# Kernel optimization log

Hardware: AMD Instinct MI355X
Metric: run time of the kernel (lower is better)

## Reference

```python
import jax, jax.numpy as jnp
import numpy as np

EMO = 1024
FEAT = 1024
K = 128  # aggregation_k
H_LIST = (4, 8, 16)
D_LIST = tuple(EMO // h for h in H_LIST)  # (256, 128, 64)
D_SUM = sum(D_LIST)  # 448
H_SUM = sum(H_LIST)  # 28
N = len(H_LIST)      # 3 subspaces
TEMP = float(np.power(D_SUM, 0.5))


def _block_mask(sizes, total):
    m = np.zeros((len(sizes), total), np.float32)
    off = 0
    for i, s in enumerate(sizes):
        m[i, off:off + s] = 1.0
        off += s
    return jnp.asarray(m)

M_Q_BLK = _block_mask(D_LIST, D_SUM)  # [N, d_sum]
M_V_BLK = _block_mask(H_LIST, H_SUM)  # [N, h_sum]


def setup_inputs() -> dict:
    key = jax.random.key(0)
    ks = iter(jax.random.split(key, 32))
    nrm = lambda shape, s=1.0: jax.random.normal(next(ks), shape, jnp.float32) * s
    B, Lt, Lp, Nv = 32, 1024, 512, 256
    return {
        "emo_embedding": nrm((B, Lt, EMO)),
        "phr_feat": nrm((B, Lp, FEAT)),
        "video_feat": nrm((B, Nv, FEAT)),
        "w_v_W": nrm((FEAT, FEAT), FEAT ** -0.5), "w_v_b": nrm((FEAT,), 0.01),
        "agg_a_W": nrm((FEAT, K), FEAT ** -0.5), "agg_a_b": nrm((K,), 0.01),
        "agg_c_W": nrm((FEAT, EMO), FEAT ** -0.5), "agg_c_b": nrm((EMO,), 0.01),
        "ele_W": nrm((2 * EMO, 1), (2 * EMO) ** -0.5), "ele_b": nrm((1,), 0.01),
        "wq_W": nrm((EMO, D_SUM), EMO ** -0.5), "wq_b": nrm((D_SUM,), 0.01),
        "wk_W": nrm((EMO, D_SUM), EMO ** -0.5), "wk_b": nrm((D_SUM,), 0.01),
        "wv_W": nrm((EMO, H_SUM), EMO ** -0.5), "wv_b": nrm((H_SUM,), 0.01),
        "wr_W": nrm((EMO, N), EMO ** -0.5), "wr_b": nrm((N,), 0.01),
    }


def reference(emo_embedding, phr_feat, video_feat,
              w_v_W, w_v_b, agg_a_W, agg_a_b, agg_c_W, agg_c_b,
              ele_W, ele_b, wq_W, wq_b, wk_W, wk_b, wv_W, wv_b, wr_W, wr_b):
    B, Lt, _ = emo_embedding.shape
    Nv = video_feat.shape[1]
    Lp = phr_feat.shape[1]

    # --- feature_aggregation ---
    # AdaptiveAvgPool1d(Nv); Lp % Nv == 0 so it is an exact reshape-mean.
    phr = phr_feat.reshape(B, Nv, Lp // Nv, FEAT).mean(axis=2)
    combine = jnp.concatenate([phr @ w_v_W + w_v_b, video_feat], axis=1)   # [B, 2*Nv, FEAT]
    attn_a = jax.nn.softmax(combine @ agg_a_W + agg_a_b, axis=-1)          # [B, 2*Nv, K]
    agg_feat = jnp.einsum('bmk,bme->bke', attn_a, combine @ agg_c_W + agg_c_b)  # [B, K, EMO]

    # --- element_routing ---
    A_pool = jnp.einsum('ble,bke->blk', emo_embedding, agg_feat).mean(axis=1)   # [B, K]
    route = jnp.einsum('bk,bke->be', A_pool, agg_feat)[:, None, :]              # [B, 1, EMO]
    route = jnp.broadcast_to(route, emo_embedding.shape)
    R_e = jnp.tanh(jnp.concatenate([emo_embedding, route], axis=-1) @ ele_W + ele_b)  # [B, Lt, 1]
    route_emo = R_e * emo_embedding                                              # [B, Lt, EMO]

    # --- subspace_routing ---
    Q = route_emo @ wq_W + wq_b        # [B, Lt, d_sum]
    Kp = agg_feat @ wk_W + wk_b        # [B, K, d_sum]
    V = agg_feat @ wv_W + wv_b         # [B, K, h_sum]
    Rp = agg_feat @ wr_W + wr_b        # [B, K, N]

    # N masked copies of Q (block subspace masks); K/R are plain repeats, V is masked.
    Qm = (Q[:, None] * M_Q_BLK[None, :, None, :]).reshape(B, N * Lt, D_SUM)
    Kf = jnp.tile(Kp, (1, N, 1))                                         # [B, N*K, d_sum]
    Vf = (V[:, None] * M_V_BLK[None, :, None, :]).reshape(B, N * K, H_SUM)
    Rf = jnp.tile(Rp, (1, N, 1))                                         # [B, N*K, N]

    attn = jax.nn.softmax(jnp.einsum('bqd,bkd->bqk', Qm, Kf) / TEMP, axis=-1)  # [B, N*Lt, N*K]
    O = jnp.tanh(attn @ Vf).reshape(B, N, Lt, H_SUM)
    O_R = (attn @ Rf).reshape(B, N, Lt, N)

    # per-subspace head gating of route_emo
    T_list = []
    hoff = 0
    for i in range(N):
        hi, di = H_LIST[i], D_LIST[i]
        ori = route_emo.reshape(B, Lt, hi, di)
        Oi = O[:, i, :, hoff:hoff + hi][..., None]      # [B, Lt, hi, 1]
        T_list.append((ori * Oi).reshape(B, Lt, EMO))
        hoff += hi
    T = jnp.stack(T_list, axis=1)                        # [B, N, Lt, EMO]

    Rdiag = jnp.stack([O_R[:, j, :, j].mean(axis=-1) for j in range(N)], axis=1)  # [B, N]
    gate = jax.nn.softmax(Rdiag, axis=-1)[:, :, None, None]
    return emo_embedding + (gate * T).sum(axis=1)
```

## Files before the change

### kernel.cpp

```cpp
#include <hip/hip_runtime.h>
#include <math.h>

typedef long long i64;
typedef __attribute__((ext_vector_type(8))) short bf16x8;
typedef __attribute__((ext_vector_type(4))) float f32x4;

#define TEMP_ISQ 0.047245559f

__device__ __forceinline__ unsigned short f2b(float x) {
  union { float f; unsigned u; } a; a.f = x;
  return (unsigned short)((a.u + 0x7fffu + ((a.u >> 16) & 1u)) >> 16);
}
__device__ __forceinline__ float b2f(unsigned short b) {
  union { float f; unsigned u; } a; a.u = ((unsigned)b) << 16; return a.f;
}

template<int BIAS, int OUTM, int RS, int BZDIV, int XMODE = 0>
__global__ __launch_bounds__(256)
void gemm_mfma(const unsigned short* __restrict__ Ab, i64 sA,
               const unsigned short* __restrict__ Bb, i64 sB,
               const float* __restrict__ bias,
               void* __restrict__ Ob, i64 sO,
               unsigned short* __restrict__ O2b, i64 sO2,
               int Nn, int Kd, int ldA, int ldB, int ldO,
               const float* __restrict__ rowScale, i64 sRS,
               const float* __restrict__ rsAdd)
{
  __shared__ unsigned short As[2][4096];
  __shared__ unsigned short Bs[2][4096];
  const int tid = threadIdx.x;
  const int w = tid >> 6, lane = tid & 63;

  const int gx = gridDim.x, gy = gridDim.y;
  int nwg = gx * gy * gridDim.z;
  int bid = blockIdx.x + gx * (blockIdx.y + gy * blockIdx.z);
  int L = bid;
  if ((nwg & 7) == 0) L = (bid & 7) * (nwg >> 3) + (bid >> 3);
  const int bx = L % gx;
  int rem = L / gx;
  const int by = rem % gy;
  const int z  = rem / gy;

  const int m0 = by * 128, n0 = bx * 128;
  int zA = (XMODE == 2) ? z / 3 : z;
  const unsigned short* A;
  const unsigned short* B;
  int KdL = Kd;
  if (XMODE == 3) {
    int bb = z / 3, ii = z - bb * 3;
    const int dof_[3] = {0, 256, 384};
    const int kdt_[3] = {256, 128, 64};
    A = Ab + (i64)bb * sA + dof_[ii];
    B = Bb + dof_[ii];
    KdL = kdt_[ii];
  } else if (XMODE == 2) {
    A = Ab + (i64)zA * sA;
    B = Bb + (i64)z * sB;
  } else {
    A = Ab + (i64)z * sA;
    B = Bb + (i64)(BZDIV == 1 ? z : z / BZDIV) * sB;
  }
  const int wr = w >> 1, wc = w & 1;
  const int rS = tid >> 2, sS = tid & 3;
  const int cL = lane & 15, sl = lane >> 4;

  f32x4 acc[4][4];
  #pragma unroll
  for (int i = 0; i < 4; ++i)
    #pragma unroll
    for (int j = 0; j < 4; ++j) acc[i][j] = (f32x4){0.f, 0.f, 0.f, 0.f};

  auto STAGE = [&](int buf, int k0) {
    #pragma unroll
    for (int q = 0; q < 2; ++q) {
      int r = rS + q * 64;
      int sg = sS ^ ((r >> 1) & 3);
      const unsigned short* sa = A + (i64)(m0 + r) * ldA + k0 + sg * 8;
      const unsigned short* sb = B + (i64)(n0 + r) * ldB + k0 + sg * 8;
      __builtin_amdgcn_global_load_lds(
          (__attribute__((address_space(1))) void*)sa,
          (__attribute__((address_space(3))) void*)&As[buf][r * 32 + sS * 8], 16, 0, 0);
      __builtin_amdgcn_global_load_lds(
          (__attribute__((address_space(1))) void*)sb,
          (__attribute__((address_space(3))) void*)&Bs[buf][r * 32 + sS * 8], 16, 0, 0);
    }
  };

  STAGE(0, 0);
  __syncthreads();

  for (int k0 = 0; k0 < KdL; k0 += 32) {
    const int cur = (k0 >> 5) & 1;
    if (k0 + 32 < KdL) STAGE(cur ^ 1, k0 + 32);
    bf16x8 af[4], bfv[4];
    #pragma unroll
    for (int mi = 0; mi < 4; ++mi) {
      int rr = wr * 64 + mi * 16 + cL;
      int ph = sl ^ ((rr >> 1) & 3);
      af[mi] = *(const bf16x8*)&As[cur][rr * 32 + ph * 8];
    }
    #pragma unroll
    for (int ni = 0; ni < 4; ++ni) {
      int rr = wc * 64 + ni * 16 + cL;
      int ph = sl ^ ((rr >> 1) & 3);
      bfv[ni] = *(const bf16x8*)&Bs[cur][rr * 32 + ph * 8];
    }
    #pragma unroll
    for (int mi = 0; mi < 4; ++mi)
      #pragma unroll
      for (int ni = 0; ni < 4; ++ni)
        acc[mi][ni] = __builtin_amdgcn_mfma_f32_16x16x32_bf16(af[mi], bfv[ni], acc[mi][ni], 0, 0, 0);
    __syncthreads();
  }

  const float* bp = (XMODE == 2) ? (bias + (i64)z * 128) : bias;
  #pragma unroll
  for (int mi = 0; mi < 4; ++mi) {
    const int rowb = m0 + wr * 64 + mi * 16 + sl * 4;
    #pragma unroll
    for (int ni = 0; ni < 4; ++ni) {
      const int col = n0 + wc * 64 + ni * 16 + cL;
      if (col < Nn) {
        float bc = (BIAS == 1) ? bp[col] : 0.f;
        #pragma unroll
        for (int rg = 0; rg < 4; ++rg) {
          float v = acc[mi][ni][rg];
          if (RS) v *= tanhf(rowScale[(i64)zA * sRS + rowb + rg] + rsAdd[zA]);
          v += bc;
          if (BIAS == 2) v += bias[rowb + rg];
          i64 oidx = (i64)(rowb + rg) * ldO + col;
          if (OUTM == 0)      ((float*)Ob)[(i64)z * sO + oidx] = v;
          else if (OUTM == 1) ((unsigned short*)Ob)[(i64)z * sO + oidx] = f2b(v);
          else if (OUTM == 4) {
            float ov = (col < 28) ? tanhf(v * (1.f / 3.f)) : v * (1.f / 1024.f);
            ((float*)Ob)[(i64)z * sO + oidx] = ov;
          } else {
            ((float*)Ob)[(i64)z * sO + oidx] = v;
            O2b[(i64)z * sO2 + oidx] = f2b(v);
          }
        }
      }
    }
  }
}

__global__ __launch_bounds__(256)
void emo_pass1(const float* __restrict__ emo, const float* __restrict__ eleW,
               unsigned short* __restrict__ emoB, float* __restrict__ colPart,
               float* __restrict__ dotE) {
  int b = blockIdx.y, lc = blockIdx.x;
  int t = threadIdx.x, lane = t & 63, w = t >> 6;
  float4 w4 = ((const float4*)eleW)[t];
  float4 acc = make_float4(0.f, 0.f, 0.f, 0.f);
  __shared__ float dw[16][4];
  const float4* src = (const float4*)emo + ((i64)b * 1024 + lc * 16) * 256;
  ushort4* dst = (ushort4*)emoB + ((i64)b * 1024 + lc * 16) * 256;
  #pragma unroll 4
  for (int lr = 0; lr < 16; ++lr) {
    float4 v = src[lr * 256 + t];
    acc.x += v.x; acc.y += v.y; acc.z += v.z; acc.w += v.w;
    float d = v.x * w4.x + v.y * w4.y + v.z * w4.z + v.w * w4.w;
    #pragma unroll
    for (int o = 32; o; o >>= 1) d += __shfl_xor(d, o);
    if (!lane) dw[lr][w] = d;
    ushort4 o4; o4.x = f2b(v.x); o4.y = f2b(v.y); o4.z = f2b(v.z); o4.w = f2b(v.w);
    dst[lr * 256 + t] = o4;
  }
  __syncthreads();
  if (t < 16) dotE[(i64)b * 1024 + lc * 16 + t] = dw[t][0] + dw[t][1] + dw[t][2] + dw[t][3];
  ((float4*)colPart)[((i64)b * 64 + lc) * 256 + t] = acc;
}

__global__ __launch_bounds__(256)
void transpose_all(const float* __restrict__ w_v_W, const float* __restrict__ agg_a_W,
                   const float* __restrict__ agg_c_W, const float* __restrict__ wq_W,
                   const float* __restrict__ wk_W, const float* __restrict__ wv_W,
                   const float* __restrict__ wr_W,
                   unsigned short* __restrict__ wvT, unsigned short* __restrict__ aaT,
                   unsigned short* __restrict__ acT, unsigned short* __restrict__ wqB,
                   unsigned short* __restrict__ kvrT) {
  int bx = blockIdx.x;
  int t = threadIdx.x;
  if (bx >= 84) {
    i64 li = (((i64)(bx - 84) * 32 + blockIdx.y) * 256 + t) * 4;
    float4 v = *(const float4*)(wq_W + li);
    ushort4 o; o.x = f2b(v.x); o.y = f2b(v.y); o.z = f2b(v.z); o.w = f2b(v.w);
    *(ushort4*)(wqB + li) = o;
    return;
  }
  __shared__ float T[32][33];
  const float* in; unsigned short* out; int N, Npad, s0;
  if (bx < 32)      { in = w_v_W;   out = wvT;                     N = 1024; Npad = 1024; s0 = 0; }
  else if (bx < 36) { in = agg_a_W; out = aaT;                     N = 128;  Npad = 128;  s0 = 32; }
  else if (bx < 68) { in = agg_c_W; out = acT;                     N = 1024; Npad = 1024; s0 = 36; }
  else if (bx < 82) { in = wk_W;    out = kvrT;                    N = 448;  Npad = 448;  s0 = 68; }
  else if (bx < 83) { in = wv_W;    out = kvrT + (i64)448 * 1024;  N = 28;   Npad = 28;   s0 = 82; }
  else              { in = wr_W;    out = kvrT + (i64)476 * 1024;  N = 3;    Npad = 36;   s0 = 83; }
  int n0 = (bx - s0) * 32, k0 = blockIdx.y * 32;
  #pragma unroll
  for (int p = 0; p < 4; ++p) {
    int idx = t + 256 * p; int kk = idx >> 5, nn = idx & 31;
    float v = 0.f;
    if (n0 + nn < N) v = in[(i64)(k0 + kk) * N + (n0 + nn)];
    T[nn][kk] = v;
  }
  __syncthreads();
  #pragma unroll
  for (int p = 0; p < 4; ++p) {
    int idx = t + 256 * p; int nn = idx >> 5, kk = idx & 31;
    if (n0 + nn < Npad) out[(i64)(n0 + nn) * 1024 + (k0 + kk)] = f2b(T[nn][kk]);
  }
}

__global__ void kvr_bias_kernel(const float* wkb, const float* wvb, const float* wrb, float* out) {
  int t = blockIdx.x * 256 + threadIdx.x;
  if (t >= 480) return;
  out[t] = (t < 448) ? wkb[t] : (t < 476) ? wvb[t - 448] : (t < 479) ? wrb[t - 476] : 0.f;
}

__global__ void pv_conv(const float* __restrict__ phr, const float* __restrict__ video,
                        unsigned short* __restrict__ pooled, unsigned short* __restrict__ combine) {
  i64 idx = (i64)blockIdx.x * 256 + threadIdx.x;
  if (idx < 2097152) {
    i64 bm = idx >> 8; int c = (int)(idx & 255);
    i64 b = bm >> 8, m = bm & 255;
    const float4* r0 = (const float4*)(phr + (b * 512 + 2 * m) * 1024) + c;
    const float4* r1 = (const float4*)(phr + (b * 512 + 2 * m + 1) * 1024) + c;
    float4 a = *r0, d = *r1;
    ushort4 o;
    o.x = f2b(0.5f * (a.x + d.x)); o.y = f2b(0.5f * (a.y + d.y));
    o.z = f2b(0.5f * (a.z + d.z)); o.w = f2b(0.5f * (a.w + d.w));
    ((ushort4*)pooled)[idx] = o;
  } else {
    i64 j = idx - 2097152;
    i64 b = j >> 16, r = j & 65535;
    float4 v = ((const float4*)video)[j];
    ushort4 o;
    o.x = f2b(v.x); o.y = f2b(v.y); o.z = f2b(v.z); o.w = f2b(v.w);
    ((ushort4*)combine)[b * 131072 + 65536 + r] = o;
  }
}

__global__ void vtq_fill(const unsigned short* __restrict__ KVR, const float* __restrict__ wq_b,
                         unsigned short* __restrict__ VT, float* __restrict__ qb) {
  int b = blockIdx.y, bx = blockIdx.x, t = threadIdx.x;
  if (bx < 64) {
    int idx = bx * 256 + t;
    int n = idx >> 7, k = idx & 127;
    unsigned short v = 0;
    if (n < 28)      v = KVR[(i64)b * 61440 + k * 480 + 448 + n];
    else if (n < 31) v = KVR[(i64)b * 61440 + k * 480 + 476 + (n - 28)];
    VT[((i64)b * 128 + n) * 128 + k] = v;
  } else if (t < 128) {
    int ii = bx - 64;
    const int dof_[3] = {0, 256, 384};
    const int kdt_[3] = {256, 128, 64};
    const unsigned short* kp = KVR + (i64)b * 61440 + t * 480 + dof_[ii];
    const float* wb = wq_b + dof_[ii];
    float s = 0.f;
    for (int d = 0; d < kdt_[ii]; ++d) s += b2f(kp[d]) * wb[d];
    qb[(b * 3 + ii) * 128 + t] = s;
  }
}

__global__ void softmax_attn_a(const float* __restrict__ logits, unsigned short* __restrict__ outT) {
  int gw = (int)(((i64)blockIdx.x * blockDim.x + threadIdx.x) >> 6);
  int lane = threadIdx.x & 63;
  if (gw >= 32 * 512) return;
  int b = gw >> 9, m = gw & 511;
  const float* p = logits + (i64)gw * 128;
  float x0 = p[lane], x1 = p[lane + 64];
  float mx = fmaxf(x0, x1);
  #pragma unroll
  for (int o = 32; o; o >>= 1) mx = fmaxf(mx, __shfl_xor(mx, o));
  float e0 = expf(x0 - mx), e1 = expf(x1 - mx);
  float s = e0 + e1;
  #pragma unroll
  for (int o = 32; o; o >>= 1) s += __shfl_xor(s, o);
  float inv = 1.f / s;
  unsigned short* o0 = outT + (i64)b * 128 * 512 + m;
  o0[(i64)lane * 512] = f2b(e0 * inv);
  o0[(i64)(lane + 64) * 512] = f2b(e1 * inv);
}

__global__ void softmax_P_bf(const unsigned short* __restrict__ PL, unsigned short* __restrict__ P) {
  i64 gw = ((i64)blockIdx.x * blockDim.x + threadIdx.x) >> 6;
  int lane = threadIdx.x & 63;
  if (gw >= 98304) return;
  const unsigned short* p = PL + gw * 128;
  float x0 = b2f(p[lane]) * TEMP_ISQ, x1 = b2f(p[lane + 64]) * TEMP_ISQ;
  float mx = fmaxf(x0, x1);
  #pragma unroll
  for (int o = 32; o; o >>= 1) mx = fmaxf(mx, __shfl_xor(mx, o));
  float e0 = expf(x0 - mx), e1 = expf(x1 - mx);
  float s = e0 + e1;
  #pragma unroll
  for (int o = 32; o; o >>= 1) s += __shfl_xor(s, o);
  float inv = 1.f / s;
  P[gw * 128 + lane] = f2b(e0 * inv);
  P[gw * 128 + lane + 64] = f2b(e1 * inv);
}

__global__ __launch_bounds__(256)
void colmean_apool(const float* __restrict__ colPart, const float* __restrict__ aggF,
                   float* __restrict__ Apool) {
  int b = blockIdx.x, t = threadIdx.x, lane = t & 63, w = t >> 6;
  __shared__ float em[1024];
  float4 s = make_float4(0.f, 0.f, 0.f, 0.f);
  const float4* cp = (const float4*)colPart + (i64)b * 64 * 256 + t;
  for (int lc = 0; lc < 64; ++lc) {
    float4 v = cp[lc * 256];
    s.x += v.x; s.y += v.y; s.z += v.z; s.w += v.w;
  }
  em[t * 4 + 0] = s.x * (1.f / 1024.f); em[t * 4 + 1] = s.y * (1.f / 1024.f);
  em[t * 4 + 2] = s.z * (1.f / 1024.f); em[t * 4 + 3] = s.w * (1.f / 1024.f);
  __syncthreads();
  for (int k = w; k < 128; k += 4) {
    const float* ag = aggF + ((i64)b * 128 + k) * 1024;
    float d = 0.f;
    #pragma unroll
    for (int j = 0; j < 16; ++j) { int e = j * 64 + lane; d += em[e] * ag[e]; }
    #pragma unroll
    for (int o = 32; o; o >>= 1) d += __shfl_down(d, o);
    if (!lane) Apool[b * 128 + k] = d;
  }
}

__global__ __launch_bounds__(256)
void route_rb(const float* __restrict__ Apool, const float* __restrict__ aggF,
              const float* __restrict__ eleW, const float* __restrict__ eleb,
              float* __restrict__ rbv) {
  int b = blockIdx.x, t = threadIdx.x;
  __shared__ float Ap[128];
  if (t < 128) Ap[t] = Apool[b * 128 + t];
  __syncthreads();
  float4 r = make_float4(0.f, 0.f, 0.f, 0.f);
  const float4* ag = (const float4*)(aggF + (i64)b * 128 * 1024) + t;
  #pragma unroll 8
  for (int k = 0; k < 128; ++k) {
    float a = Ap[k];
    float4 v = ag[(i64)k * 256];
    r.x += a * v.x; r.y += a * v.y; r.z += a * v.z; r.w += a * v.w;
  }
  float4 w4 = ((const float4*)(eleW + 1024))[t];
  float d = r.x * w4.x + r.y * w4.y + r.z * w4.z + r.w * w4.w;
  __shared__ float red[256];
  red[t] = d; __syncthreads();
  for (int o = 128; o > 0; o >>= 1) { if (t < o) red[t] += red[t + o]; __syncthreads(); }
  if (t == 0) rbv[b] = red[0] + eleb[0];
}

__global__ void gate_kernel(const float* __restrict__ O, float* __restrict__ gate) {
  int b = blockIdx.x, t = threadIdx.x;
  __shared__ float red[128];
  __shared__ float rd[3];
  for (int i = 0; i < 3; ++i) {
    const float* op = O + ((i64)(b * 3 + i) * 1024) * 32 + 28 + i;
    float s = 0.f;
    #pragma unroll
    for (int l = t; l < 1024; l += 128) s += op[(i64)l * 32];
    red[t] = s; __syncthreads();
    for (int o = 64; o > 0; o >>= 1) { if (t < o) red[t] += red[t + o]; __syncthreads(); }
    if (t == 0) rd[i] = red[0];
    __syncthreads();
  }
  if (t == 0) {
    float m = fmaxf(rd[0], fmaxf(rd[1], rd[2]));
    float e0 = expf(rd[0] - m), e1 = expf(rd[1] - m), e2 = expf(rd[2] - m);
    float inv = 1.f / (e0 + e1 + e2);
    gate[b * 3 + 0] = e0 * inv; gate[b * 3 + 1] = e1 * inv; gate[b * 3 + 2] = e2 * inv;
  }
}

__global__ __launch_bounds__(256)
void final_kernel(const unsigned short* __restrict__ emoB, const float* __restrict__ dotE,
                  const float* __restrict__ rbv, const float* __restrict__ O,
                  const float* __restrict__ gate, float* __restrict__ out) {
  i64 bl = blockIdx.x;
  int b = (int)(bl >> 10), l = (int)(bl & 1023);
  __shared__ float Gg[16];
  int t = threadIdx.x;
  if (t < 16) {
    float g0 = gate[b * 3], g1 = gate[b * 3 + 1], g2 = gate[b * 3 + 2];
    float o0 = O[((i64)(b * 3 + 0) * 1024 + l) * 32 + (t >> 2)];
    float o1 = O[((i64)(b * 3 + 1) * 1024 + l) * 32 + 4 + (t >> 1)];
    float o2 = O[((i64)(b * 3 + 2) * 1024 + l) * 32 + 12 + t];
    Gg[t] = g0 * o0 + g1 * o1 + g2 * o2;
  }
  __syncthreads();
  float re = tanhf(dotE[bl] + rbv[b]);
  ushort4 e4 = ((const ushort4*)(emoB + bl * 1024))[t];
  float g = 1.f + re * Gg[t >> 4];
  ((float4*)(out + bl * 1024))[t] =
      make_float4(b2f(e4.x) * g, b2f(e4.y) * g, b2f(e4.z) * g, b2f(e4.w) * g);
}

extern "C" void kernel_launch(void* const* d_in, const int* in_sizes, int n_in,
                              void* d_out, int out_size, void* d_ws, size_t ws_size,
                              hipStream_t stream) {
  const float* emo     = (const float*)d_in[0];
  const float* phr     = (const float*)d_in[1];
  const float* video   = (const float*)d_in[2];
  const float* w_v_W   = (const float*)d_in[3];
  const float* w_v_b   = (const float*)d_in[4];
  const float* agg_a_W = (const float*)d_in[5];
  const float* agg_a_b = (const float*)d_in[6];
  const float* agg_c_W = (const float*)d_in[7];
  const float* agg_c_b = (const float*)d_in[8];
  const float* ele_W   = (const float*)d_in[9];
  const float* ele_b   = (const float*)d_in[10];
  const float* wq_W    = (const float*)d_in[11];
  const float* wq_b    = (const float*)d_in[12];
  const float* wk_W    = (const float*)d_in[13];
  const float* wk_b    = (const float*)d_in[14];
  const float* wv_W    = (const float*)d_in[15];
  const float* wv_b    = (const float*)d_in[16];
  const float* wr_W    = (const float*)d_in[17];
  const float* wr_b    = (const float*)d_in[18];

  char* ws = (char*)d_ws;
  const i64 oEmoB    = 0;
  const i64 oCombine = 67108864;
  const i64 oP       = 67108864;
  const i64 oPooled  = 100663296;
  const i64 oLogitsA = 100663296;
  const i64 oAggF    = 100663296;
  const i64 oO       = 100663296;
  const i64 oCT      = 117440512;
  const i64 oW2T     = 117440512;
  const i64 oAttnAT  = 150994944;
  const i64 oAggB    = 155189248;
  const i64 oWvT     = 163577856;
  const i64 oAaT     = 165675008;
  const i64 oAcT     = 165937152;
  const i64 oWqB     = 168034304;
  const i64 oKvrT    = 169082880;
  const i64 oKVR     = 170131456;
  const i64 oVT      = 174063616;
  const i64 oKvrB    = 175112192;
  const i64 oColPart = 175247360;
  const i64 oDotE    = 183635968;
  const i64 oApool   = 183767040;
  const i64 oQb      = 183783424;
  const i64 oRb      = 183914496;
  const i64 oGate    = 184307968;

  unsigned short* emoB    = (unsigned short*)(ws + oEmoB);
  unsigned short* combine = (unsigned short*)(ws + oCombine);
  unsigned short* P       = (unsigned short*)(ws + oP);
  unsigned short* pooled  = (unsigned short*)(ws + oPooled);
  float*          logitsA = (float*)(ws + oLogitsA);
  float*          aggF    = (float*)(ws + oAggF);
  float*          O       = (float*)(ws + oO);
  unsigned short* CT      = (unsigned short*)(ws + oCT);
  unsigned short* W2T     = (unsigned short*)(ws + oW2T);
  unsigned short* attnAT  = (unsigned short*)(ws + oAttnAT);
  unsigned short* aggB    = (unsigned short*)(ws + oAggB);
  unsigned short* wvT     = (unsigned short*)(ws + oWvT);
  unsigned short* aaT     = (unsigned short*)(ws + oAaT);
  unsigned short* acT     = (unsigned short*)(ws + oAcT);
  unsigned short* wqB     = (unsigned short*)(ws + oWqB);
  unsigned short* kvrT    = (unsigned short*)(ws + oKvrT);
  unsigned short* KVR     = (unsigned short*)(ws + oKVR);
  unsigned short* VT      = (unsigned short*)(ws + oVT);
  float*          kvrB    = (float*)(ws + oKvrB);
  float*          colPart = (float*)(ws + oColPart);
  float*          dotE    = (float*)(ws + oDotE);
  float*          Apool   = (float*)(ws + oApool);
  float*          qb      = (float*)(ws + oQb);
  float*          rbv     = (float*)(ws + oRb);
  float*          gate    = (float*)(ws + oGate);

  dim3 blk(256);

  emo_pass1<<<dim3(64, 32), blk, 0, stream>>>(emo, ele_W, emoB, colPart, dotE);

  transpose_all<<<dim3(98, 32), blk, 0, stream>>>(w_v_W, agg_a_W, agg_c_W, wq_W, wk_W, wv_W, wr_W,
                                                  wvT, aaT, acT, wqB, kvrT);
  kvr_bias_kernel<<<2, blk, 0, stream>>>(wk_b, wv_b, wr_b, kvrB);

  pv_conv<<<16384, blk, 0, stream>>>(phr, video, pooled, combine);
  gemm_mfma<1, 1, 0, 1><<<dim3(8, 2, 32), blk, 0, stream>>>(pooled, 262144, wvT, 0, w_v_b,
      (void*)combine, 524288, nullptr, 0, 1024, 1024, 1024, 1024, 1024, nullptr, 0, nullptr);
  gemm_mfma<1, 0, 0, 1><<<dim3(1, 4, 32), blk, 0, stream>>>(combine, 524288, aaT, 0, agg_a_b,
      (void*)logitsA, 65536, nullptr, 0, 128, 1024, 1024, 1024, 128, nullptr, 0, nullptr);
  softmax_attn_a<<<4096, blk, 0, stream>>>(logitsA, attnAT);
  gemm_mfma<2, 1, 0, 1><<<dim3(4, 8, 32), blk, 0, stream>>>(acT, 0, combine, 524288, agg_c_b,
      (void*)CT, 524288, nullptr, 0, 512, 1024, 1024, 1024, 512, nullptr, 0, nullptr);
  gemm_mfma<0, 2, 0, 1><<<dim3(8, 1, 32), blk, 0, stream>>>(attnAT, 65536, CT, 524288, nullptr,
      (void*)aggF, 131072, aggB, 131072, 1024, 512, 512, 512, 1024, nullptr, 0, nullptr);

  colmean_apool<<<32, blk, 0, stream>>>(colPart, aggF, Apool);
  route_rb<<<32, blk, 0, stream>>>(Apool, aggF, ele_W, ele_b, rbv);

  gemm_mfma<1, 1, 0, 1><<<dim3(4, 1, 32), blk, 0, stream>>>(aggB, 131072, kvrT, 0, kvrB,
      (void*)KVR, 61440, nullptr, 0, 480, 1024, 1024, 1024, 480, nullptr, 0, nullptr);
  vtq_fill<<<dim3(67, 32), blk, 0, stream>>>(KVR, wq_b, VT, qb);

  gemm_mfma<0, 1, 0, 1, 3><<<dim3(8, 1, 96), blk, 0, stream>>>(KVR, 61440, wqB, 0, nullptr,
      (void*)W2T, 131072, nullptr, 0, 1024, 0, 480, 448, 1024, nullptr, 0, nullptr);

  gemm_mfma<1, 1, 1, 1, 2><<<dim3(1, 8, 96), blk, 0, stream>>>(emoB, 1048576, W2T, 131072, qb,
      (void*)P, 131072, nullptr, 0, 128, 1024, 1024, 1024, 128, dotE, 1024, rbv);

  softmax_P_bf<<<24576, blk, 0, stream>>>(P, P);

  gemm_mfma<0, 4, 0, 3><<<dim3(1, 8, 96), blk, 0, stream>>>(P, 131072, VT, 16384, nullptr,
      (void*)O, 32768, nullptr, 0, 31, 128, 128, 128, 32, nullptr, 0, nullptr);

  gate_kernel<<<32, 128, 0, stream>>>(O, gate);
  final_kernel<<<32768, blk, 0, stream>>>(emoB, dotE, rbv, O, gate, (float*)d_out);
}
```

Measured before the change: 458.1 us.

## Reassociate aggregation einsum to apply attention before the agg_c projection

Computes agg_feat as (attn_a^T @ combine) @ agg_c_W + colsum(attn_a) * agg_c_b instead of attn_a^T @ (combine @ agg_c_W + b). This shrinks the large projection GEMM from 512 rows per batch to 128 rows per batch. To support it, the change adds a combine transpose kernel, a column-sum kernel for the bias term, and a new BIAS mode that scales the bias by a per-row factor. The intermediate S1 is rounded to bf16, which slightly changes numerics.

Measured after the change: 450.8 us (median of 2 runs). No clear change (-1.6%).

```diff
diff --git a/kernel.cpp b/kernel.cpp
--- a/kernel.cpp
+++ b/kernel.cpp
@@ -128,6 +128,7 @@
           if (RS) v *= tanhf(rowScale[(i64)zA * sRS + rowb + rg] + rsAdd[zA]);
           v += bc;
           if (BIAS == 2) v += bias[rowb + rg];
+          if (BIAS == 3) v += rowScale[(i64)z * sRS + rowb + rg] * bp[col];
           i64 oidx = (i64)(rowb + rg) * ldO + col;
           if (OUTM == 0)      ((float*)Ob)[(i64)z * sO + oidx] = v;
           else if (OUTM == 1) ((unsigned short*)Ob)[(i64)z * sO + oidx] = f2b(v);
@@ -239,6 +240,41 @@
     o.x = f2b(v.x); o.y = f2b(v.y); o.z = f2b(v.z); o.w = f2b(v.w);
     ((ushort4*)combine)[b * 131072 + 65536 + r] = o;
   }
+}
+
+__global__ __launch_bounds__(256)
+void combT_kernel(const unsigned short* __restrict__ in, unsigned short* __restrict__ out) {
+  __shared__ unsigned short T[64][68];
+  int b = blockIdx.z, mt = blockIdx.y, ft = blockIdx.x;
+  int t = threadIdx.x;
+  const unsigned short* src = in + (i64)b * 524288 + (i64)(mt * 64) * 1024 + ft * 64;
+  unsigned short* dst = out + (i64)b * 524288 + (i64)(ft * 64) * 512 + mt * 64;
+  int r0 = t >> 4, c4 = (t & 15) * 4;
+  #pragma unroll
+  for (int p = 0; p < 4; ++p) {
+    int r = r0 + p * 16;
+    ushort4 v = *(const ushort4*)&src[(i64)r * 1024 + c4];
+    T[r][c4] = v.x; T[r][c4 + 1] = v.y; T[r][c4 + 2] = v.z; T[r][c4 + 3] = v.w;
+  }
+  __syncthreads();
+  #pragma unroll
+  for (int p = 0; p < 4; ++p) {
+    int fr = r0 + p * 16;
+    ushort4 v;
+    v.x = T[c4][fr]; v.y = T[c4 + 1][fr]; v.z = T[c4 + 2][fr]; v.w = T[c4 + 3][fr];
+    *(ushort4*)&dst[(i64)fr * 512 + c4] = v;
+  }
+}
+
+__global__ void colsum_kernel(const unsigned short* __restrict__ attnAT, float* __restrict__ colsum) {
+  int b = blockIdx.x, k = threadIdx.x;
+  const ushort4* p = (const ushort4*)(attnAT + ((i64)b * 128 + k) * 512);
+  float s = 0.f;
+  for (int m4 = 0; m4 < 128; ++m4) {
+    ushort4 v = p[m4];
+    s += b2f(v.x) + b2f(v.y) + b2f(v.z) + b2f(v.w);
+  }
+  colsum[b * 128 + k] = s;
 }
 
 __global__ void vtq_fill(const unsigned short* __restrict__ KVR, const float* __restrict__ wq_b,
@@ -421,6 +457,7 @@
   char* ws = (char*)d_ws;
   const i64 oEmoB    = 0;
   const i64 oCombine = 67108864;
+  const i64 oS1B     = 67108864;
   const i64 oP       = 67108864;
   const i64 oPooled  = 100663296;
   const i64 oLogitsA = 100663296;
@@ -444,15 +481,17 @@
   const i64 oQb      = 183783424;
   const i64 oRb      = 183914496;
   const i64 oGate    = 184307968;
+  const i64 oColsum  = 184308480;
 
   unsigned short* emoB    = (unsigned short*)(ws + oEmoB);
   unsigned short* combine = (unsigned short*)(ws + oCombine);
+  unsigned short* S1B     = (unsigned short*)(ws + oS1B);
   unsigned short* P       = (unsigned short*)(ws + oP);
   unsigned short* pooled  = (unsigned short*)(ws + oPooled);
   float*          logitsA = (float*)(ws + oLogitsA);
   float*          aggF    = (float*)(ws + oAggF);
   float*          O       = (float*)(ws + oO);
-  unsigned short* CT      = (unsigned short*)(ws + oCT);
+  unsigned short* combineT= (unsigned short*)(ws + oCT);
   unsigned short* W2T     = (unsigned short*)(ws + oW2T);
   unsigned short* attnAT  = (unsigned short*)(ws + oAttnAT);
   unsigned short* aggB    = (unsigned short*)(ws + oAggB);
@@ -470,6 +509,7 @@
   float*          qb      = (float*)(ws + oQb);
   float*          rbv     = (float*)(ws + oRb);
   float*          gate    = (float*)(ws + oGate);
+  float*          colsum  = (float*)(ws + oColsum);
 
   dim3 blk(256);
 
@@ -485,10 +525,13 @@
   gemm_mfma<1, 0, 0, 1><<<dim3(1, 4, 32), blk, 0, stream>>>(combine, 524288, aaT, 0, agg_a_b,
       (void*)logitsA, 65536, nullptr, 0, 128, 1024, 1024, 1024, 128, nullptr, 0, nullptr);
   softmax_attn_a<<<4096, blk, 0, stream>>>(logitsA, attnAT);
-  gemm_mfma<2, 1, 0, 1><<<dim3(4, 8, 32), blk, 0, stream>>>(acT, 0, combine, 524288, agg_c_b,
-      (void*)CT, 524288, nullptr, 0, 512, 1024, 1024, 1024, 512, nullptr, 0, nullptr);
-  gemm_mfma<0, 2, 0, 1><<<dim3(8, 1, 32), blk, 0, stream>>>(attnAT, 65536, CT, 524288, nullptr,
-      (void*)aggF, 131072, aggB, 131072, 1024, 512, 512, 512, 1024, nullptr, 0, nullptr);
+  colsum_kernel<<<32, 128, 0, stream>>>(attnAT, colsum);
+  combT_kernel<<<dim3(16, 8, 32), blk, 0, stream>>>(combine, combineT);
+
+  gemm_mfma<0, 1, 0, 1><<<dim3(8, 1, 32), blk, 0, stream>>>(attnAT, 65536, combineT, 524288, nullptr,
+      (void*)S1B, 131072, nullptr, 0, 1024, 512, 512, 512, 1024, nullptr, 0, nullptr);
+  gemm_mfma<3, 2, 0, 1><<<dim3(8, 1, 32), blk, 0, stream>>>(S1B, 131072, acT, 0, agg_c_b,
+      (void*)aggF, 131072, aggB, 131072, 1024, 1024, 1024, 1024, 1024, colsum, 128, nullptr);
 
   colmean_apool<<<32, blk, 0, stream>>>(colPart, aggF, Apool);
   route_rb<<<32, blk, 0, stream>>>(Apool, aggF, ele_W, ele_b, rbv);
```
